# Performance work log

Measured on AMD Instinct MI355X. Metric: run time of the kernel, lower is better.

## Reference

```python
import jax, jax.numpy as jnp
import numpy as np

N_NODES = 100000
N_FEATURES = 128
N_FILTERS = 128
N_EDGES = 3200000


def setup_inputs() -> dict:
    key = jax.random.key(0)
    k_x, k_f, k_src, k_dst, k_w = jax.random.split(key, 5)
    x = jax.random.normal(k_x, (N_NODES, N_FEATURES), dtype=jnp.float32)
    filters = jax.random.normal(k_f, (N_FEATURES, N_FILTERS), dtype=jnp.float32)
    edge_src = jax.random.randint(k_src, (N_EDGES,), 0, N_NODES, dtype=jnp.int64)
    edge_dst = jnp.sort(jax.random.randint(k_dst, (N_EDGES,), 0, N_NODES, dtype=jnp.int64))
    edge_weight = jax.random.uniform(k_w, (N_EDGES,), dtype=jnp.float32)
    return {"x": x, "filters": filters, "edge_src": edge_src,
            "edge_dst": edge_dst, "edge_weight": edge_weight}


def reference(x, filters, edge_src, edge_dst, edge_weight):
    # Dense feature transform: XF = x @ filters  -> [N, n_filters]
    XF = jnp.matmul(x, filters)
    # Sparse aggregation: out[d] += w_e * XF[s] for each edge (s, d, w_e)
    # equivalent to torch.sparse.mm(transform, XF) with transform in COO form.
    msgs = XF[edge_src] * edge_weight[:, None]           # [E, n_filters]
    out = jax.ops.segment_sum(msgs, edge_dst, num_segments=N_NODES)
    return out
```

## Files before the change

### kernel.cpp

```cpp
#include <hip/hip_runtime.h>
#include <stdint.h>

#define N_NODES 100000
#define N_FEAT 128
#define N_EDGES 3200000

static __device__ __forceinline__ unsigned int f2bf_u(float f) {
    unsigned int u = __float_as_uint(f);
    u += 0x7FFFu + ((u >> 16) & 1u);
    return u >> 16;
}

typedef __bf16 bf16x8 __attribute__((ext_vector_type(8)));
typedef float f32x4 __attribute__((ext_vector_type(4)));

__global__ __launch_bounds__(256) void k_prep(
        const float* __restrict__ f, unsigned short* __restrict__ fB,
        const int* __restrict__ dst, int* __restrict__ row_ptr) {
    int b = blockIdx.x;
    if (b < 12500) {
        int e = b * 256 + threadIdx.x;
        if (e >= N_EDGES) return;
        int dcur = dst[e];
        if (e == 0) {
            for (int d = 0; d <= dcur; ++d) row_ptr[d] = 0;
        } else {
            int dprev = dst[e - 1];
            for (int d = dprev + 1; d <= dcur; ++d) row_ptr[d] = e;
        }
        if (e == N_EDGES - 1) {
            for (int d = dcur + 1; d <= N_NODES; ++d) row_ptr[d] = N_EDGES;
        }
    } else {
        int i = (b - 12500) * 256 + threadIdx.x;
        if (i >= N_FEAT * N_FEAT) return;
        int n = ((i >> 11) << 4) | ((i >> 3) & 15);
        int k = (((i >> 9) & 3) << 5) | (((i >> 7) & 3) << 3) | (i & 7);
        fB[i] = (unsigned short)f2bf_u(f[k * 128 + n]);
    }
}

__global__ __launch_bounds__(256) void k_xf(
        const float* __restrict__ x,
        const unsigned short* __restrict__ fB,
        unsigned int* __restrict__ xi8,
        float* __restrict__ xscale) {
    __shared__ unsigned short Bbuf[16384];
    int t = threadIdx.x;
    for (int i = 0; i < 8; ++i)
        ((uint4*)Bbuf)[t + i * 256] = ((const uint4*)fB)[t + i * 256];
    __syncthreads();

    int wave = t >> 6, lane = t & 63, m15 = lane & 15, q = lane >> 4;
    int row = blockIdx.x * 64 + wave * 16 + m15;
    int rowc = min(row, N_NODES - 1);

    f32x4 acc[8];
#pragma unroll
    for (int j = 0; j < 8; ++j) acc[j] = f32x4{0.f, 0.f, 0.f, 0.f};

#pragma unroll
    for (int kkidx = 0; kkidx < 4; ++kkidx) {
        const float* ap = x + (size_t)rowc * 128 + kkidx * 32 + q * 8;
        float4 v0 = *(const float4*)ap;
        float4 v1 = *(const float4*)(ap + 4);
        union { bf16x8 v; unsigned short s[8]; } au;
        au.s[0] = (unsigned short)f2bf_u(v0.x);
        au.s[1] = (unsigned short)f2bf_u(v0.y);
        au.s[2] = (unsigned short)f2bf_u(v0.z);
        au.s[3] = (unsigned short)f2bf_u(v0.w);
        au.s[4] = (unsigned short)f2bf_u(v1.x);
        au.s[5] = (unsigned short)f2bf_u(v1.y);
        au.s[6] = (unsigned short)f2bf_u(v1.z);
        au.s[7] = (unsigned short)f2bf_u(v1.w);
#pragma unroll
        for (int j = 0; j < 8; ++j) {
            bf16x8 bfrag = *(const bf16x8*)(Bbuf + (((j * 4 + kkidx) * 64 + lane) * 8));
            acc[j] = __builtin_amdgcn_mfma_f32_16x16x32_bf16(au.v, bfrag, acc[j], 0, 0, 0);
        }
    }

    int rowbase = blockIdx.x * 64 + wave * 16 + q * 4;
#pragma unroll
    for (int r = 0; r < 4; ++r) {
        float mx = 0.f;
#pragma unroll
        for (int j = 0; j < 8; ++j) mx = fmaxf(mx, fabsf(acc[j][r]));
        for (int d = 1; d < 16; d <<= 1) mx = fmaxf(mx, __shfl_xor(mx, d));
        float inv = 127.f / fmaxf(mx, 1e-20f);
        unsigned int u0 = 0, u1 = 0;
#pragma unroll
        for (int bb = 0; bb < 4; ++bb) {
            unsigned int q0 = (unsigned int)(int)(rintf(acc[2 * bb][r] * inv) + 128.f);
            unsigned int q1 = (unsigned int)(int)(rintf(acc[2 * bb + 1][r] * inv) + 128.f);
            u0 |= (q0 & 0xFFu) << (8 * bb);
            u1 |= (q1 & 0xFFu) << (8 * bb);
        }
        int gr = rowbase + r;
        if (gr < N_NODES) {
            xi8[(size_t)gr * 32 + m15] = u0;
            xi8[(size_t)gr * 32 + 16 + m15] = u1;
            if (m15 == 0) xscale[gr] = mx * (1.f / 127.f);
        }
    }
}

__global__ __launch_bounds__(256) void k_aggregate(
        const unsigned int* __restrict__ xi8,
        const float* __restrict__ xscale,
        const int* __restrict__ src,
        const float* __restrict__ w,
        const int* __restrict__ row_ptr,
        float* __restrict__ out) {
    __shared__ uint2 smeta[4][64];
    int wave = threadIdx.x >> 6, lane = threadIdx.x & 63;
    int node = blockIdx.x * 4 + wave;
    if (node >= N_NODES) return;
    int g8 = lane >> 3, l8 = lane & 7;
    unsigned int bo = (unsigned int)(l8 * 16);
    int start = row_ptr[node], end = row_ptr[node + 1];
    uint2* sm = smeta[wave];
    const char* xb = (const char*)xi8;

    f32x4 acc[4];
#pragma unroll
    for (int b = 0; b < 4; ++b) acc[b] = f32x4{0.f, 0.f, 0.f, 0.f};
    float aw = 0.f;

#define FMAU(QQ, CC) do {                                                    \
        acc[0][CC] = fmaf(wu_, (float)( (QQ)        & 0xFFu), acc[0][CC]);   \
        acc[1][CC] = fmaf(wu_, (float)(((QQ) >>  8) & 0xFFu), acc[1][CC]);   \
        acc[2][CC] = fmaf(wu_, (float)(((QQ) >> 16) & 0xFFu), acc[2][CC]);   \
        acc[3][CC] = fmaf(wu_, (float)( (QQ) >> 24         ), acc[3][CC]);   \
    } while (0)
#define FMAG(V, WUU) do { float wu_ = __uint_as_float(WUU);                  \
        FMAU((V).x, 0); FMAU((V).y, 1); FMAU((V).z, 2); FMAU((V).w, 3);      \
    } while (0)

    for (int e0 = start; e0 < end; e0 += 64) {
        int e = e0 + lane;
        uint2 m = make_uint2(0u, 0u);
        if (e < end) {
            int sv = src[e];
            m.x = (unsigned int)sv << 7;
            m.y = __float_as_uint(w[e] * xscale[sv]);
        }
        sm[lane] = m;
        aw += __uint_as_float(m.y);
        int ng = (min(64, end - e0) + 7) >> 3;
        uint2 mm0 = sm[g8];
        uint4 v0 = *(const uint4*)(xb + (mm0.x + bo));
        for (int j = 0; j + 1 < ng; ++j) {
            uint2 mm1 = sm[(j + 1) * 8 + g8];
            uint4 v1 = *(const uint4*)(xb + (mm1.x + bo));
            FMAG(v0, mm0.y);
            mm0 = mm1; v0 = v1;
        }
        FMAG(v0, mm0.y);
    }
#undef FMAU
#undef FMAG

#pragma unroll
    for (int b = 0; b < 4; ++b)
#pragma unroll
        for (int cc = 0; cc < 4; ++cc) {
            float v = acc[b][cc];
            v += __shfl_xor(v, 8);
            v += __shfl_xor(v, 16);
            v += __shfl_xor(v, 32);
            acc[b][cc] = v;
        }
    aw += __shfl_xor(aw, 1);
    aw += __shfl_xor(aw, 2);
    aw += __shfl_xor(aw, 4);
    aw += __shfl_xor(aw, 8);
    aw += __shfl_xor(aw, 16);
    aw += __shfl_xor(aw, 32);

    if (g8 == 0) {
        float* o = out + (size_t)node * 128 + l8 * 4;
#pragma unroll
        for (int b = 0; b < 4; ++b) {
            float4 ov;
            ov.x = fmaf(-128.f, aw, acc[b][0]);
            ov.y = fmaf(-128.f, aw, acc[b][1]);
            ov.z = fmaf(-128.f, aw, acc[b][2]);
            ov.w = fmaf(-128.f, aw, acc[b][3]);
            *(float4*)(o + b * 32) = ov;
        }
    }
}

extern "C" void kernel_launch(void* const* d_in, const int* in_sizes, int n_in,
                              void* d_out, int out_size, void* d_ws, size_t ws_size,
                              hipStream_t stream) {
    const float* x        = (const float*)d_in[0];
    const float* filters  = (const float*)d_in[1];
    const int*   edge_src = (const int*)d_in[2];
    const int*   edge_dst = (const int*)d_in[3];
    const float* edge_w   = (const float*)d_in[4];
    float* out = (float*)d_out;

    char* ws = (char*)d_ws;
    unsigned int*   xi8 = (unsigned int*)  (ws);
    float*          xsc = (float*)         (ws + 13ll * 1024 * 1024);
    unsigned short* fB  = (unsigned short*)(ws + 14ll * 1024 * 1024);
    int*            rp  = (int*)           (ws + 15ll * 1024 * 1024);

    hipLaunchKernelGGL(k_prep, dim3(12564), dim3(256), 0, stream,
                       filters, fB, edge_dst, rp);
    hipLaunchKernelGGL(k_xf, dim3(1563), dim3(256), 0, stream,
                       x, fB, xi8, xsc);
    hipLaunchKernelGGL(k_aggregate, dim3(25000), dim3(256), 0, stream,
                       xi8, xsc, edge_src, edge_w, rp, out);
}
```

Measured before the change: 200.9 us.

## Split quantized features into four column slices and aggregate each slice separately

The int8 transformed features are stored as four column slices of 32 bytes per node, and the aggregation grid is multiplied by four so each block handles one slice for four nodes. Each lane now gathers 4 bytes instead of 16, so the gathered working set of each slice is a quarter of the full array and is meant to stay in cache. Edge loads and output stores use nontemporal hints. In exchange, src, weight and xscale are read four times, the gathers are narrower, and the block count rises to 100000.

```diff
diff --git a/kernel.cpp b/kernel.cpp
--- a/kernel.cpp
+++ b/kernel.cpp
@@ -4,6 +4,7 @@
 #define N_NODES 100000
 #define N_FEAT 128
 #define N_EDGES 3200000
+#define SLICE_U 800000
 
 static __device__ __forceinline__ unsigned int f2bf_u(float f) {
     unsigned int u = __float_as_uint(f);
@@ -98,8 +99,9 @@
         }
         int gr = rowbase + r;
         if (gr < N_NODES) {
-            xi8[(size_t)gr * 32 + m15] = u0;
-            xi8[(size_t)gr * 32 + 16 + m15] = u1;
+            int s0 = m15 >> 3, p0 = m15 & 7;
+            xi8[s0 * SLICE_U + gr * 8 + p0] = u0;
+            xi8[(2 + s0) * SLICE_U + gr * 8 + p0] = u1;
             if (m15 == 0) xscale[gr] = mx * (1.f / 127.f);
         }
     }
@@ -114,63 +116,56 @@
         float* __restrict__ out) {
     __shared__ uint2 smeta[4][64];
     int wave = threadIdx.x >> 6, lane = threadIdx.x & 63;
-    int node = blockIdx.x * 4 + wave;
+    int s = blockIdx.x & 3;
+    int node = (blockIdx.x >> 2) * 4 + wave;
     if (node >= N_NODES) return;
     int g8 = lane >> 3, l8 = lane & 7;
-    unsigned int bo = (unsigned int)(l8 * 16);
+    unsigned int lo4 = (unsigned int)(l8 * 4);
+    const char* xb = (const char*)(xi8 + (size_t)s * SLICE_U);
     int start = row_ptr[node], end = row_ptr[node + 1];
     uint2* sm = smeta[wave];
-    const char* xb = (const char*)xi8;
-
-    f32x4 acc[4];
-#pragma unroll
-    for (int b = 0; b < 4; ++b) acc[b] = f32x4{0.f, 0.f, 0.f, 0.f};
+
+    f32x4 acc = f32x4{0.f, 0.f, 0.f, 0.f};
     float aw = 0.f;
-
-#define FMAU(QQ, CC) do {                                                    \
-        acc[0][CC] = fmaf(wu_, (float)( (QQ)        & 0xFFu), acc[0][CC]);   \
-        acc[1][CC] = fmaf(wu_, (float)(((QQ) >>  8) & 0xFFu), acc[1][CC]);   \
-        acc[2][CC] = fmaf(wu_, (float)(((QQ) >> 16) & 0xFFu), acc[2][CC]);   \
-        acc[3][CC] = fmaf(wu_, (float)( (QQ) >> 24         ), acc[3][CC]);   \
-    } while (0)
-#define FMAG(V, WUU) do { float wu_ = __uint_as_float(WUU);                  \
-        FMAU((V).x, 0); FMAU((V).y, 1); FMAU((V).z, 2); FMAU((V).w, 3);      \
-    } while (0)
 
     for (int e0 = start; e0 < end; e0 += 64) {
         int e = e0 + lane;
         uint2 m = make_uint2(0u, 0u);
         if (e < end) {
-            int sv = src[e];
-            m.x = (unsigned int)sv << 7;
-            m.y = __float_as_uint(w[e] * xscale[sv]);
+            int sv = __builtin_nontemporal_load(src + e);
+            m.x = (unsigned int)sv << 5;
+            m.y = __float_as_uint(__builtin_nontemporal_load(w + e) * xscale[sv]);
         }
         sm[lane] = m;
         aw += __uint_as_float(m.y);
-        int ng = (min(64, end - e0) + 7) >> 3;
-        uint2 mm0 = sm[g8];
-        uint4 v0 = *(const uint4*)(xb + (mm0.x + bo));
-        for (int j = 0; j + 1 < ng; ++j) {
-            uint2 mm1 = sm[(j + 1) * 8 + g8];
-            uint4 v1 = *(const uint4*)(xb + (mm1.x + bo));
-            FMAG(v0, mm0.y);
-            mm0 = mm1; v0 = v1;
-        }
-        FMAG(v0, mm0.y);
-    }
-#undef FMAU
-#undef FMAG
-
-#pragma unroll
-    for (int b = 0; b < 4; ++b)
-#pragma unroll
-        for (int cc = 0; cc < 4; ++cc) {
-            float v = acc[b][cc];
-            v += __shfl_xor(v, 8);
-            v += __shfl_xor(v, 16);
-            v += __shfl_xor(v, 32);
-            acc[b][cc] = v;
-        }
+        int nj4 = ((min(64, end - e0) + 31) >> 5) << 2;
+        for (int j0 = 0; j0 < nj4; j0 += 4) {
+            unsigned int vv[4]; float wj[4];
+#pragma unroll
+            for (int u = 0; u < 4; ++u) {
+                uint2 mm = sm[(j0 + u) * 8 + g8];
+                wj[u] = __uint_as_float(mm.y);
+                vv[u] = *(const unsigned int*)(xb + (mm.x + lo4));
+            }
+#pragma unroll
+            for (int u = 0; u < 4; ++u) {
+                unsigned int v = vv[u]; float wu = wj[u];
+                acc[0] = fmaf(wu, (float)( v        & 0xFFu), acc[0]);
+                acc[1] = fmaf(wu, (float)((v >>  8) & 0xFFu), acc[1]);
+                acc[2] = fmaf(wu, (float)((v >> 16) & 0xFFu), acc[2]);
+                acc[3] = fmaf(wu, (float)( v >> 24         ), acc[3]);
+            }
+        }
+    }
+
+#pragma unroll
+    for (int cc = 0; cc < 4; ++cc) {
+        float v = acc[cc];
+        v += __shfl_xor(v, 8);
+        v += __shfl_xor(v, 16);
+        v += __shfl_xor(v, 32);
+        acc[cc] = v;
+    }
     aw += __shfl_xor(aw, 1);
     aw += __shfl_xor(aw, 2);
     aw += __shfl_xor(aw, 4);
@@ -179,16 +174,11 @@
     aw += __shfl_xor(aw, 32);
 
     if (g8 == 0) {
-        float* o = out + (size_t)node * 128 + l8 * 4;
-#pragma unroll
-        for (int b = 0; b < 4; ++b) {
-            float4 ov;
-            ov.x = fmaf(-128.f, aw, acc[b][0]);
-            ov.y = fmaf(-128.f, aw, acc[b][1]);
-            ov.z = fmaf(-128.f, aw, acc[b][2]);
-            ov.w = fmaf(-128.f, aw, acc[b][3]);
-            *(float4*)(o + b * 32) = ov;
-        }
+        float* o = out + (size_t)node * 128 + s * 8 + l8;
+        __builtin_nontemporal_store(fmaf(-128.f, aw, acc[0]), o);
+        __builtin_nontemporal_store(fmaf(-128.f, aw, acc[1]), o + 32);
+        __builtin_nontemporal_store(fmaf(-128.f, aw, acc[2]), o + 64);
+        __builtin_nontemporal_store(fmaf(-128.f, aw, acc[3]), o + 96);
     }
 }
 
@@ -204,14 +194,14 @@
 
     char* ws = (char*)d_ws;
     unsigned int*   xi8 = (unsigned int*)  (ws);
-    float*          xsc = (float*)         (ws + 13ll * 1024 * 1024);
-    unsigned short* fB  = (unsigned short*)(ws + 14ll * 1024 * 1024);
-    int*            rp  = (int*)           (ws + 15ll * 1024 * 1024);
+    float*          xsc = (float*)         (ws + 13000000);
+    int*            rp  = (int*)           (ws + 13500000);
+    unsigned short* fB  = (unsigned short*)(ws + 14000000);
 
     hipLaunchKernelGGL(k_prep, dim3(12564), dim3(256), 0, stream,
                        filters, fB, edge_dst, rp);
     hipLaunchKernelGGL(k_xf, dim3(1563), dim3(256), 0, stream,
                        x, fB, xi8, xsc);
-    hipLaunchKernelGGL(k_aggregate, dim3(25000), dim3(256), 0, stream,
+    hipLaunchKernelGGL(k_aggregate, dim3(25000 * 4), dim3(256), 0, stream,
                        xi8, xsc, edge_src, edge_w, rp, out);
 }
```

Result: slower. 319.3 us (+58.9%).
